# Kernel optimization log

Hardware: AMD Instinct MI355X
Metric: run time of the kernel (lower is better)

Reference implementation:

```python
import jax, jax.numpy as jnp
import numpy as np

DIM = 3072
KV_DIM = 2048
HEADS = 16
DIM_HEAD = 128
INNER = HEADS * DIM_HEAD  # 2048
EPS = 1e-5


def layer_norm(x, g, b):
    mu = jnp.mean(x, axis=-1, keepdims=True)
    var = jnp.mean(jnp.square(x - mu), axis=-1, keepdims=True)
    return (x - mu) * jax.lax.rsqrt(var + EPS) * g + b


def setup_inputs() -> dict:
    key = jax.random.key(0)
    ks = jax.random.split(key, 7)
    B, SQ, SKV = 2, 2048, 1024
    image_embeds = jax.random.normal(ks[0], (B, SKV, KV_DIM), dtype=jnp.float32)
    hidden_states = jax.random.normal(ks[1], (B, SQ, DIM), dtype=jnp.float32)
    Wq = jax.random.normal(ks[2], (DIM, INNER), dtype=jnp.float32) * (DIM ** -0.5)
    Wkv = jax.random.normal(ks[3], (KV_DIM, 2 * INNER), dtype=jnp.float32) * (KV_DIM ** -0.5)
    Wout = jax.random.normal(ks[4], (INNER, DIM), dtype=jnp.float32) * (INNER ** -0.5)
    ln1_g = jnp.ones((KV_DIM,), jnp.float32)
    ln1_b = jnp.zeros((KV_DIM,), jnp.float32)
    ln2_g = jnp.ones((DIM,), jnp.float32)
    ln2_b = jnp.zeros((DIM,), jnp.float32)
    return dict(image_embeds=image_embeds, hidden_states=hidden_states,
                Wq=Wq, Wkv=Wkv, Wout=Wout,
                ln1_g=ln1_g, ln1_b=ln1_b, ln2_g=ln2_g, ln2_b=ln2_b)


def reference(image_embeds, hidden_states, Wq, Wkv, Wout, ln1_g, ln1_b, ln2_g, ln2_b):
    x_kv = layer_norm(image_embeds, ln1_g, ln1_b)   # [B, Skv, kv_dim]
    x_q = layer_norm(hidden_states, ln2_g, ln2_b)   # [B, Sq, dim]
    B, SQ, _ = x_q.shape
    q = x_q @ Wq                                    # [B, Sq, inner]
    kv = x_kv @ Wkv                                 # [B, Skv, 2*inner]
    k, v = jnp.split(kv, 2, axis=-1)
    # [B, H, S, Dh]
    q = q.reshape(B, SQ, HEADS, DIM_HEAD).transpose(0, 2, 1, 3)
    k = k.reshape(B, -1, HEADS, DIM_HEAD).transpose(0, 2, 1, 3)
    v = v.reshape(B, -1, HEADS, DIM_HEAD).transpose(0, 2, 1, 3)
    scale = 1.0 / np.sqrt(np.sqrt(DIM_HEAD)).astype(np.float32)
    # scale applied to both q and k, as in the original (q*s) @ (k*s)^T
    logits = jnp.einsum('bhqd,bhkd->bhqk', q * scale, k * scale)
    weight = jax.nn.softmax(logits.astype(jnp.float32), axis=-1).astype(logits.dtype)
    out = jnp.einsum('bhqk,bhkd->bhqd', weight, v)  # [B, H, Sq, Dh]
    out = out.transpose(0, 2, 1, 3).reshape(B, SQ, INNER)
    return out @ Wout
```

## Files before the change

kernel.cpp:

```cpp
#include <hip/hip_runtime.h>
#include <hip/hip_bf16.h>

typedef unsigned short u16;
typedef __attribute__((ext_vector_type(8))) __bf16 bf16x8;
typedef __attribute__((ext_vector_type(4))) float f32x4;
typedef __attribute__((ext_vector_type(2))) unsigned int u32x2;

#define DEV __device__ __forceinline__

DEV u16 f2bf(float f) {
  union { float f; unsigned int u; } v; v.f = f;
  unsigned int x = v.u;
  return (u16)((x + 0x7fffu + ((x >> 16) & 1u)) >> 16);
}

DEV void gload_lds16(const u16* g, u16* l) {
  __builtin_amdgcn_global_load_lds(
      (__attribute__((address_space(1))) void*)(g),
      (__attribute__((address_space(3))) void*)(l), 16, 0, 0);
}

template <int NV>
DEV void ln_body(const float* x, const float* g, const float* b, u16* out,
                 int C, int row, float* red) {
  int tid = threadIdx.x;
  const float4* xr = (const float4*)(x + (size_t)row * C);
  float4 v[NV];
  float s = 0.f, ss = 0.f;
#pragma unroll
  for (int i = 0; i < NV; i++) {
    v[i] = xr[tid + i * 256];
    s += v[i].x + v[i].y + v[i].z + v[i].w;
    ss += v[i].x * v[i].x + v[i].y * v[i].y + v[i].z * v[i].z + v[i].w * v[i].w;
  }
#pragma unroll
  for (int off = 32; off > 0; off >>= 1) {
    s += __shfl_down(s, off);
    ss += __shfl_down(ss, off);
  }
  int wv = tid >> 6;
  if ((tid & 63) == 0) { red[wv] = s; red[4 + wv] = ss; }
  __syncthreads();
  float S = red[0] + red[1] + red[2] + red[3];
  float SS = red[4] + red[5] + red[6] + red[7];
  float mu = S / C;
  float rstd = rsqrtf(SS / C - mu * mu + 1e-5f);
  const float4* gr = (const float4*)g;
  const float4* br = (const float4*)b;
  ushort4* orow = (ushort4*)(out + (size_t)row * C);
#pragma unroll
  for (int i = 0; i < NV; i++) {
    int gi = tid + i * 256;
    float4 gv = gr[gi], bv = br[gi];
    ushort4 o;
    o.x = f2bf((v[i].x - mu) * rstd * gv.x + bv.x);
    o.y = f2bf((v[i].y - mu) * rstd * gv.y + bv.y);
    o.z = f2bf((v[i].z - mu) * rstd * gv.z + bv.z);
    o.w = f2bf((v[i].w - mu) * rstd * gv.w + bv.w);
    orow[gi] = o;
  }
}

DEV void tr_body(const float* in, u16* out, int K, int N, int bx, int by,
                 float (*t)[33]) {
  int tx = threadIdx.x & 31, ty = threadIdx.x >> 5;
  int n0 = bx * 32, k0 = by * 32;
#pragma unroll
  for (int i = 0; i < 32; i += 8)
    t[ty + i][tx] = in[(size_t)(k0 + ty + i) * N + n0 + tx];
  __syncthreads();
#pragma unroll
  for (int i = 0; i < 32; i += 8)
    out[(size_t)(n0 + ty + i) * K + k0 + tx] = f2bf(t[tx][ty + i]);
}

__global__ __launch_bounds__(256) void prep(
    const float* __restrict__ hidden, const float* __restrict__ image,
    const float* __restrict__ Wq, const float* __restrict__ Wkv,
    const float* __restrict__ Wout,
    const float* __restrict__ ln1_g, const float* __restrict__ ln1_b,
    const float* __restrict__ ln2_g, const float* __restrict__ ln2_b,
    u16* __restrict__ Xq, u16* __restrict__ Xkv,
    u16* __restrict__ WqT, u16* __restrict__ WkvT, u16* __restrict__ WoT) {
  __shared__ float t[32][33];
  int i = blockIdx.x;
  if (i < 4096) {
    ln_body<3>(hidden, ln2_g, ln2_b, Xq, 3072, i, &t[0][0]);
  } else if (i < 6144) {
    ln_body<2>(image, ln1_g, ln1_b, Xkv, 2048, i - 4096, &t[0][0]);
  } else if (i < 12288) {
    int j = i - 6144;
    tr_body(Wq, WqT, 3072, 2048, j & 63, j >> 6, t);
  } else if (i < 20480) {
    int j = i - 12288;
    tr_body(Wkv, WkvT, 2048, 4096, j & 127, j >> 7, t);
  } else {
    int j = i - 20480;
    tr_body(Wout, WoT, 2048, 3072, j % 96, j / 96, t);
  }
}

__global__ __launch_bounds__(256) void build_vt(const u16* __restrict__ KV,
                                                u16* __restrict__ VT) {
  __shared__ u16 t[32][33];
  int bh = blockIdx.z, b = bh >> 4, h = bh & 15;
  int d0 = blockIdx.x * 32, s0 = blockIdx.y * 32;
  int tx = threadIdx.x & 31, ty = threadIdx.x >> 5;
  const u16* src = KV + (size_t)(b * 1024) * 4096 + 2048 + h * 128;
#pragma unroll
  for (int i = 0; i < 32; i += 8)
    t[ty + i][tx] = src[(size_t)(s0 + ty + i) * 4096 + d0 + tx];
  __syncthreads();
  u16* dst = VT + (size_t)bh * (128 * 1024);
#pragma unroll
  for (int i = 0; i < 32; i += 8) {
    int d = d0 + ty + i;
    int kv = s0 + tx;
    int c = kv >> 6, w = kv & 63;
    int s = (w >> 3) ^ (d & 7), e = w & 7;
    dst[c * 8192 + d * 64 + s * 8 + e] = t[tx][ty + i];
  }
}

DEV void storeC(u16* C, size_t idx, float v) { C[idx] = f2bf(v); }
DEV void storeC(float* C, size_t idx, float v) { C[idx] = v; }

#define MFMA16(a, b, c) __builtin_amdgcn_mfma_f32_16x16x32_bf16((a), (b), (c), 0, 0, 0)

template <typename OutT>
__global__ __launch_bounds__(512, 2) void gemm8(
    const u16* __restrict__ Aa, const u16* __restrict__ Ba, OutT* __restrict__ Ca,
    int Na, int Ka, float osa,
    const u16* __restrict__ Ab2, const u16* __restrict__ Bb2, OutT* __restrict__ Cb2,
    int Nb, int Kb, float osb, int nblk0) {
  __shared__ __attribute__((aligned(16))) u16 Alds[2][256 * 64];
  __shared__ __attribute__((aligned(16))) u16 Blds[2][256 * 64];

  int nwg = gridDim.x;
  int bid = ((int)blockIdx.x & 7) * (nwg >> 3) + ((int)blockIdx.x >> 3);

  const u16* A; const u16* B; OutT* C; int N, K; float oscale;
  if (bid < nblk0) { A = Aa; B = Ba; C = Ca; N = Na; K = Ka; oscale = osa; }
  else { bid -= nblk0; A = Ab2; B = Bb2; C = Cb2; N = Nb; K = Kb; oscale = osb; }

  int tilesN = N >> 8;
  int bm = (bid / tilesN) << 8;
  int bn = (bid % tilesN) << 8;
  int tid = threadIdx.x, lane = tid & 63, w = tid >> 6;
  int wr = w >> 2, wc = w & 3;
  int fr = lane & 15, g = lane >> 4;
  const u16* Abase = A + (size_t)bm * K;
  const u16* Bbase = B + (size_t)bn * K;

  int lrow = lane >> 3;
  int lcol = (((lane & 7) ^ lrow) << 3);

  auto stageA = [&](int kt, int unit, int bufb) {
#pragma unroll
    for (int j = 0; j < 2; j++) {
      int bi = w * 2 + j;
      int r0 = ((bi >> 3) << 7) + (unit << 6) + ((bi & 7) << 3);
      gload_lds16(Abase + (size_t)(r0 + lrow) * K + kt + lcol,
                  &Alds[bufb][r0 * 64]);
    }
  };
  auto stageB = [&](int kt, int unit, int bufb) {
#pragma unroll
    for (int j = 0; j < 2; j++) {
      int bi = w * 2 + j;
      int r0 = ((bi >> 2) << 6) + (unit << 5) + ((bi & 3) << 3);
      gload_lds16(Bbase + (size_t)(r0 + lrow) * K + kt + lcol,
                  &Blds[bufb][r0 * 64]);
    }
  };
  auto rdA = [&](int bufb, int m, int kk) {
    int row = (wr << 7) + m * 16 + fr;
    int slot = (kk * 4 + g) ^ (fr & 7);
    return *(const bf16x8*)&Alds[bufb][row * 64 + slot * 8];
  };
  auto rdB = [&](int bufb, int n, int kk) {
    int row = (wc << 6) + n * 16 + fr;
    int slot = (kk * 4 + g) ^ (fr & 7);
    return *(const bf16x8*)&Blds[bufb][row * 64 + slot * 8];
  };

  f32x4 acc[8][4] = {};
  const int NT = K >> 6;

  stageA(0, 0, 0); stageB(0, 0, 0); stageB(0, 1, 0); stageA(0, 1, 0);
  stageA(64, 0, 1); stageB(64, 0, 1); stageB(64, 1, 1);
  asm volatile("s_waitcnt vmcnt(6)" ::: "memory");
  __builtin_amdgcn_sched_barrier(0);
  __builtin_amdgcn_s_barrier();

  bf16x8 af[4][2], bf0[2][2], bf1[2][2];
  for (int X = 0; X < NT; ++X) {
    int cur = X & 1, nxt = cur ^ 1;

#pragma unroll
    for (int m = 0; m < 4; m++) { af[m][0] = rdA(cur, m, 0); af[m][1] = rdA(cur, m, 1); }
#pragma unroll
    for (int n = 0; n < 2; n++) { bf0[n][0] = rdB(cur, n, 0); bf0[n][1] = rdB(cur, n, 1); }
    if (X + 1 < NT) stageA((X + 1) << 6, 1, nxt);
    __builtin_amdgcn_s_setprio(1);
#pragma unroll
    for (int m = 0; m < 4; m++)
#pragma unroll
      for (int n = 0; n < 2; n++) {
        acc[m][n] = MFMA16(af[m][0], bf0[n][0], acc[m][n]);
        acc[m][n] = MFMA16(af[m][1], bf0[n][1], acc[m][n]);
      }
    __builtin_amdgcn_s_setprio(0);
    __builtin_amdgcn_s_barrier();

#pragma unroll
    for (int n = 0; n < 2; n++) { bf1[n][0] = rdB(cur, n + 2, 0); bf1[n][1] = rdB(cur, n + 2, 1); }
    if (X + 2 < NT) stageA((X + 2) << 6, 0, cur);
    __builtin_amdgcn_s_setprio(1);
#pragma unroll
    for (int m = 0; m < 4; m++)
#pragma unroll
      for (int n = 0; n < 2; n++) {
        acc[m][n + 2] = MFMA16(af[m][0], bf1[n][0], acc[m][n + 2]);
        acc[m][n + 2] = MFMA16(af[m][1], bf1[n][1], acc[m][n + 2]);
      }
    __builtin_amdgcn_s_setprio(0);
    __builtin_amdgcn_s_barrier();

#pragma unroll
    for (int m = 0; m < 4; m++) { af[m][0] = rdA(cur, m + 4, 0); af[m][1] = rdA(cur, m + 4, 1); }
    if (X + 2 < NT) stageB((X + 2) << 6, 0, cur);
    __builtin_amdgcn_s_setprio(1);
#pragma unroll
    for (int m = 0; m < 4; m++)
#pragma unroll
      for (int n = 0; n < 2; n++) {
        acc[m + 4][n] = MFMA16(af[m][0], bf0[n][0], acc[m + 4][n]);
        acc[m + 4][n] = MFMA16(af[m][1], bf0[n][1], acc[m + 4][n]);
      }
    __builtin_amdgcn_s_setprio(0);
    __builtin_amdgcn_s_barrier();

    if (X + 2 < NT) stageB((X + 2) << 6, 1, cur);
    __builtin_amdgcn_s_setprio(1);
#pragma unroll
    for (int m = 0; m < 4; m++)
#pragma unroll
      for (int n = 0; n < 2; n++) {
        acc[m + 4][n + 2] = MFMA16(af[m][0], bf1[n][0], acc[m + 4][n + 2]);
        acc[m + 4][n + 2] = MFMA16(af[m][1], bf1[n][1], acc[m + 4][n + 2]);
      }
    __builtin_amdgcn_s_setprio(0);
    if (X + 2 < NT) {
      asm volatile("s_waitcnt vmcnt(6)" ::: "memory");
    } else {
      asm volatile("s_waitcnt vmcnt(0)" ::: "memory");
    }
    __builtin_amdgcn_sched_barrier(0);
    __builtin_amdgcn_s_barrier();
  }

#pragma unroll
  for (int m = 0; m < 8; m++) {
    int rbase = bm + (wr << 7) + m * 16 + g * 4;
#pragma unroll
    for (int n = 0; n < 4; n++) {
      int col = bn + (wc << 6) + n * 16 + fr;
#pragma unroll
      for (int r = 0; r < 4; r++)
        storeC(C, (size_t)(rbase + r) * N + col, acc[m][n][r] * oscale);
    }
  }
}

__global__ __launch_bounds__(256) void attn_kernel(const u16* __restrict__ Q,
                                                   const u16* __restrict__ KV,
                                                   const u16* __restrict__ VTt,
                                                   u16* __restrict__ O) {
  const int SQ = 2048, SKV = 1024;
  const int NCHUNK = SKV / 64;
  int qt = blockIdx.x & 15, bh = blockIdx.x >> 4;
  int b = bh >> 4, h = bh & 15;
  int wave = threadIdx.x >> 6, lane = threadIdx.x & 63;
  int q0 = qt * 128 + wave * 32;
  int fr = lane & 15, g = lane >> 4, fkb = g * 8;

  __shared__ __attribute__((aligned(16))) u16 Ks[2][64 * 128];
  __shared__ __attribute__((aligned(16))) u16 Vs[128 * 64];
  __shared__ __attribute__((aligned(16))) u16 Pb[4][32 * 72];
  u16* P = &Pb[wave][0];

  bf16x8 qf[2][4];
#pragma unroll
  for (int gq = 0; gq < 2; gq++) {
    const u16* Qbase = Q + (size_t)(b * SQ + q0 + gq * 16 + fr) * 2048 + h * 128;
#pragma unroll
    for (int kd = 0; kd < 4; kd++)
      qf[gq][kd] = *(const bf16x8*)(Qbase + kd * 32 + fkb);
  }

  const u16* Kb = KV + (size_t)(b * SKV) * 4096 + h * 128;
  const u16* Vt = VTt + (size_t)bh * (128 * 1024);

  auto stageK = [&](int c, int buf) {
#pragma unroll
    for (int j = 0; j < 4; j++) {
      int r = wave * 16 + j * 4 + g;
      int gb = (lane & 15) ^ (r & 7);
      gload_lds16(Kb + (size_t)(c * 64 + r) * 4096 + gb * 8,
                  &Ks[buf][(wave * 16 + j * 4) * 128]);
    }
  };
  auto stageV = [&](int c) {
#pragma unroll
    for (int j = 0; j < 4; j++) {
      int blk = wave * 4 + j;
      gload_lds16(Vt + (size_t)c * 8192 + blk * 512 + lane * 8, &Vs[blk * 512]);
    }
  };

  f32x4 o[2][8] = {};
  float mrun[2] = {-1e30f, -1e30f};
  float lrun[2] = {0.f, 0.f};

  stageK(0, 0);
  int buf = 0;

  for (int c = 0; c < NCHUNK; c++) {
    stageV(c);
    stageK((c + 1) & 15, buf ^ 1);
    asm volatile("s_waitcnt vmcnt(8)" ::: "memory");
    __builtin_amdgcn_s_barrier();

    f32x4 acc[2][4] = {};
#pragma unroll
    for (int kv_t = 0; kv_t < 4; kv_t++) {
      int row = kv_t * 16 + fr;
#pragma unroll
      for (int kd = 0; kd < 4; kd++) {
        int pb = (kd * 4 + g) ^ (fr & 7);
        bf16x8 kf = *(const bf16x8*)&Ks[buf][row * 128 + pb * 8];
        acc[0][kv_t] = MFMA16(kf, qf[0][kd], acc[0][kv_t]);
        acc[1][kv_t] = MFMA16(kf, qf[1][kd], acc[1][kv_t]);
      }
    }

    float corr[2];
#pragma unroll
    for (int q_t = 0; q_t < 2; q_t++) {
      float pm = fmaxf(fmaxf(fmaxf(acc[q_t][0][0], acc[q_t][0][1]), fmaxf(acc[q_t][0][2], acc[q_t][0][3])),
                       fmaxf(fmaxf(acc[q_t][1][0], acc[q_t][1][1]), fmaxf(acc[q_t][1][2], acc[q_t][1][3])));
      pm = fmaxf(pm, fmaxf(fmaxf(fmaxf(acc[q_t][2][0], acc[q_t][2][1]), fmaxf(acc[q_t][2][2], acc[q_t][2][3])),
                           fmaxf(fmaxf(acc[q_t][3][0], acc[q_t][3][1]), fmaxf(acc[q_t][3][2], acc[q_t][3][3]))));
      pm = fmaxf(pm, __shfl_xor(pm, 16));
      pm = fmaxf(pm, __shfl_xor(pm, 32));
      float mn = fmaxf(mrun[q_t], pm);
      corr[q_t] = __expf(mrun[q_t] - mn);
      mrun[q_t] = mn;
      float psum = 0.f;
#pragma unroll
      for (int kv_t = 0; kv_t < 4; kv_t++) {
        float p0 = __expf(acc[q_t][kv_t][0] - mn);
        float p1 = __expf(acc[q_t][kv_t][1] - mn);
        float p2 = __expf(acc[q_t][kv_t][2] - mn);
        float p3 = __expf(acc[q_t][kv_t][3] - mn);
        psum += (p0 + p1) + (p2 + p3);
        union { __hip_bfloat162 h; unsigned int u; } lo, hi;
        lo.h = __float22bfloat162_rn(make_float2(p0, p1));
        hi.h = __float22bfloat162_rn(make_float2(p2, p3));
        u32x2 wv = {lo.u, hi.u};
        *(u32x2*)&P[(q_t * 16 + fr) * 72 + kv_t * 16 + g * 4] = wv;
      }
      lrun[q_t] = lrun[q_t] * corr[q_t] + psum;
    }

    float corr_o[2][4];
#pragma unroll
    for (int gq = 0; gq < 2; gq++)
#pragma unroll
      for (int r = 0; r < 4; r++)
        corr_o[gq][r] = __shfl(corr[gq], g * 4 + r);
#pragma unroll
    for (int gq = 0; gq < 2; gq++)
#pragma unroll
      for (int nn = 0; nn < 8; nn++) {
        o[gq][nn][0] *= corr_o[gq][0]; o[gq][nn][1] *= corr_o[gq][1];
        o[gq][nn][2] *= corr_o[gq][2]; o[gq][nn][3] *= corr_o[gq][3];
      }

    asm volatile("s_waitcnt vmcnt(4) lgkmcnt(0)" ::: "memory");
    __builtin_amdgcn_s_barrier();

    {
      bf16x8 pa00 = *(const bf16x8*)&P[fr * 72 + fkb];
      bf16x8 pa10 = *(const bf16x8*)&P[(16 + fr) * 72 + fkb];
      bf16x8 pa01 = *(const bf16x8*)&P[fr * 72 + 32 + fkb];
      bf16x8 pa11 = *(const bf16x8*)&P[(16 + fr) * 72 + 32 + fkb];
      int sw = fr & 7;
#pragma unroll
      for (int nn = 0; nn < 8; nn++) {
        int rowb = (nn * 16 + fr) * 64;
        bf16x8 v0 = *(const bf16x8*)&Vs[rowb + ((g ^ sw) << 3)];
        bf16x8 v1 = *(const bf16x8*)&Vs[rowb + (((4 + g) ^ sw) << 3)];
        o[0][nn] = MFMA16(pa00, v0, o[0][nn]);
        o[1][nn] = MFMA16(pa10, v0, o[1][nn]);
        o[0][nn] = MFMA16(pa01, v1, o[0][nn]);
        o[1][nn] = MFMA16(pa11, v1, o[1][nn]);
      }
    }

    __builtin_amdgcn_s_barrier();
    buf ^= 1;
  }
  asm volatile("s_waitcnt vmcnt(0)" ::: "memory");

#pragma unroll
  for (int q_t = 0; q_t < 2; q_t++) {
    float lt = lrun[q_t];
    lt += __shfl_xor(lt, 16);
    lt += __shfl_xor(lt, 32);
    lrun[q_t] = lt;
  }
#pragma unroll
  for (int gq = 0; gq < 2; gq++)
#pragma unroll
    for (int r = 0; r < 4; r++) {
      float lt = __shfl(lrun[gq], g * 4 + r);
      float inv = 1.0f / lt;
      int row = b * SQ + q0 + gq * 16 + g * 4 + r;
      u16* Or = O + (size_t)row * 2048 + h * 128;
#pragma unroll
      for (int nn = 0; nn < 8; nn++) Or[nn * 16 + fr] = f2bf(o[gq][nn][r] * inv);
    }
}

extern "C" void kernel_launch(void* const* d_in, const int* in_sizes, int n_in,
                              void* d_out, int out_size, void* d_ws, size_t ws_size,
                              hipStream_t stream) {
  const float* image_embeds  = (const float*)d_in[0];
  const float* hidden_states = (const float*)d_in[1];
  const float* Wq   = (const float*)d_in[2];
  const float* Wkv  = (const float*)d_in[3];
  const float* Wout = (const float*)d_in[4];
  const float* ln1_g = (const float*)d_in[5];
  const float* ln1_b = (const float*)d_in[6];
  const float* ln2_g = (const float*)d_in[7];
  const float* ln2_b = (const float*)d_in[8];
  float* out = (float*)d_out;

  char* ws = (char*)d_ws;
  size_t off = 0;
  auto alloc = [&](size_t bytes) {
    void* p = ws + off;
    off += (bytes + 255) & ~(size_t)255;
    return p;
  };
  u16* Xq   = (u16*)alloc((size_t)4096 * 3072 * 2);
  u16* Xkv  = (u16*)alloc((size_t)2048 * 2048 * 2);
  u16* WqT  = (u16*)alloc((size_t)2048 * 3072 * 2);
  u16* WkvT = (u16*)alloc((size_t)4096 * 2048 * 2);
  u16* WoT  = (u16*)alloc((size_t)3072 * 2048 * 2);
  u16* Qb   = (u16*)alloc((size_t)4096 * 2048 * 2);
  u16* KVb  = (u16*)alloc((size_t)2048 * 4096 * 2);
  u16* VTb  = WqT;
  u16* AO   = Xq;

  const float qscale = 0.08838834764831845f;

  prep<<<26624, 256, 0, stream>>>(hidden_states, image_embeds, Wq, Wkv, Wout,
                                  ln1_g, ln1_b, ln2_g, ln2_b,
                                  Xq, Xkv, WqT, WkvT, WoT);

  gemm8<u16><<<256, 512, 0, stream>>>(
      Xq, WqT, Qb, 2048, 3072, qscale,
      Xkv, WkvT, KVb, 4096, 2048, 1.0f, 128);

  build_vt<<<dim3(4, 32, 32), 256, 0, stream>>>(KVb, VTb);
  attn_kernel<<<512, 256, 0, stream>>>(Qb, KVb, VTb, AO);

  gemm8<float><<<192, 512, 0, stream>>>(
      AO, WoT, out, 3072, 2048, 1.0f,
      AO, WoT, out, 3072, 2048, 1.0f, 192);
}
```

Before: 249.7 us.

## Prefetch next K-tile fragments from LDS during last MFMA phase of GEMM

Restructures the 8-wave GEMM main loop so the A/B register fragments for the next K-tile are read from LDS during the final MFMA quadrant of the current one, and are preloaded before the loop. A separate afB register set holds the second half of the A rows. The vmcnt wait and barrier move earlier to ensure the next buffer is resident before these reads. The aim is to hide LDS read latency at the start of each iteration, at the cost of more VGPRs and a wait placed earlier in the iteration.

```diff
diff --git a/kernel.cpp b/kernel.cpp
--- a/kernel.cpp
+++ b/kernel.cpp
@@ -193,70 +193,77 @@
   __builtin_amdgcn_sched_barrier(0);
   __builtin_amdgcn_s_barrier();
 
-  bf16x8 af[4][2], bf0[2][2], bf1[2][2];
+  bf16x8 afA[4][2], afB[4][2], bf0[2][2], bf1[2][2];
+#pragma unroll
+  for (int m = 0; m < 4; m++) { afA[m][0] = rdA(0, m, 0); afA[m][1] = rdA(0, m, 1); }
+#pragma unroll
+  for (int n = 0; n < 2; n++) { bf0[n][0] = rdB(0, n, 0); bf0[n][1] = rdB(0, n, 1); }
+
   for (int X = 0; X < NT; ++X) {
     int cur = X & 1, nxt = cur ^ 1;
 
 #pragma unroll
-    for (int m = 0; m < 4; m++) { af[m][0] = rdA(cur, m, 0); af[m][1] = rdA(cur, m, 1); }
-#pragma unroll
-    for (int n = 0; n < 2; n++) { bf0[n][0] = rdB(cur, n, 0); bf0[n][1] = rdB(cur, n, 1); }
+    for (int n = 0; n < 2; n++) { bf1[n][0] = rdB(cur, n + 2, 0); bf1[n][1] = rdB(cur, n + 2, 1); }
     if (X + 1 < NT) stageA((X + 1) << 6, 1, nxt);
     __builtin_amdgcn_s_setprio(1);
 #pragma unroll
     for (int m = 0; m < 4; m++)
 #pragma unroll
       for (int n = 0; n < 2; n++) {
-        acc[m][n] = MFMA16(af[m][0], bf0[n][0], acc[m][n]);
-        acc[m][n] = MFMA16(af[m][1], bf0[n][1], acc[m][n]);
+        acc[m][n] = MFMA16(afA[m][0], bf0[n][0], acc[m][n]);
+        acc[m][n] = MFMA16(afA[m][1], bf0[n][1], acc[m][n]);
       }
     __builtin_amdgcn_s_setprio(0);
     __builtin_amdgcn_s_barrier();
 
 #pragma unroll
-    for (int n = 0; n < 2; n++) { bf1[n][0] = rdB(cur, n + 2, 0); bf1[n][1] = rdB(cur, n + 2, 1); }
+    for (int m = 0; m < 4; m++) { afB[m][0] = rdA(cur, m + 4, 0); afB[m][1] = rdA(cur, m + 4, 1); }
     if (X + 2 < NT) stageA((X + 2) << 6, 0, cur);
     __builtin_amdgcn_s_setprio(1);
 #pragma unroll
     for (int m = 0; m < 4; m++)
 #pragma unroll
       for (int n = 0; n < 2; n++) {
-        acc[m][n + 2] = MFMA16(af[m][0], bf1[n][0], acc[m][n + 2]);
-        acc[m][n + 2] = MFMA16(af[m][1], bf1[n][1], acc[m][n + 2]);
+        acc[m][n + 2] = MFMA16(afA[m][0], bf1[n][0], acc[m][n + 2]);
+        acc[m][n + 2] = MFMA16(afA[m][1], bf1[n][1], acc[m][n + 2]);
       }
     __builtin_amdgcn_s_setprio(0);
     __builtin_amdgcn_s_barrier();
 
-#pragma unroll
-    for (int m = 0; m < 4; m++) { af[m][0] = rdA(cur, m + 4, 0); af[m][1] = rdA(cur, m + 4, 1); }
     if (X + 2 < NT) stageB((X + 2) << 6, 0, cur);
     __builtin_amdgcn_s_setprio(1);
 #pragma unroll
     for (int m = 0; m < 4; m++)
 #pragma unroll
       for (int n = 0; n < 2; n++) {
-        acc[m + 4][n] = MFMA16(af[m][0], bf0[n][0], acc[m + 4][n]);
-        acc[m + 4][n] = MFMA16(af[m][1], bf0[n][1], acc[m + 4][n]);
+        acc[m + 4][n] = MFMA16(afB[m][0], bf0[n][0], acc[m + 4][n]);
+        acc[m + 4][n] = MFMA16(afB[m][1], bf0[n][1], acc[m + 4][n]);
       }
     __builtin_amdgcn_s_setprio(0);
-    __builtin_amdgcn_s_barrier();
-
+    if (X + 2 < NT) {
+      asm volatile("s_waitcnt vmcnt(4)" ::: "memory");
+    } else {
+      asm volatile("s_waitcnt vmcnt(0)" ::: "memory");
+    }
+    __builtin_amdgcn_sched_barrier(0);
+    __builtin_amdgcn_s_barrier();
+
+    if (X + 1 < NT) {
+#pragma unroll
+      for (int m = 0; m < 4; m++) { afA[m][0] = rdA(nxt, m, 0); afA[m][1] = rdA(nxt, m, 1); }
+#pragma unroll
+      for (int n = 0; n < 2; n++) { bf0[n][0] = rdB(nxt, n, 0); bf0[n][1] = rdB(nxt, n, 1); }
+    }
     if (X + 2 < NT) stageB((X + 2) << 6, 1, cur);
     __builtin_amdgcn_s_setprio(1);
 #pragma unroll
     for (int m = 0; m < 4; m++)
 #pragma unroll
       for (int n = 0; n < 2; n++) {
-        acc[m + 4][n + 2] = MFMA16(af[m][0], bf1[n][0], acc[m + 4][n + 2]);
-        acc[m + 4][n + 2] = MFMA16(af[m][1], bf1[n][1], acc[m + 4][n + 2]);
+        acc[m + 4][n + 2] = MFMA16(afB[m][0], bf1[n][0], acc[m + 4][n + 2]);
+        acc[m + 4][n + 2] = MFMA16(afB[m][1], bf1[n][1], acc[m + 4][n + 2]);
       }
     __builtin_amdgcn_s_setprio(0);
-    if (X + 2 < NT) {
-      asm volatile("s_waitcnt vmcnt(6)" ::: "memory");
-    } else {
-      asm volatile("s_waitcnt vmcnt(0)" ::: "memory");
-    }
-    __builtin_amdgcn_sched_barrier(0);
     __builtin_amdgcn_s_barrier();
   }
 
```

Measured after the change: 267.9 us. +7.3%, slower.
